# Optimization experiments

Hardware: AMD Instinct MI355X
Metric: run time of the kernel (lower is better)

## Reference

```python
import jax, jax.numpy as jnp
import numpy as np

D_MODEL = 1024
N_HEADS = 16
HEAD_DIM = D_MODEL // N_HEADS
FFN_DIM = 4096
N_EXPERTS = 8
CAP_FRAC = 0.25          # moe_eval_capacity_token_fraction (eval mode)
MOE_TOKEN_DROPOUT = 0.2  # eval: expert output scaled by (1 - p)
LN_EPS = 1e-5
B, S = 4, 512


def setup_inputs():
    key = jax.random.key(0)
    ks = jax.random.split(key, 20)
    def w(k, shape, scale=0.02):
        return jax.random.normal(k, shape, jnp.float32) * scale
    return {
        "x": jax.random.normal(ks[0], (B, S, D_MODEL), jnp.float32),
        "wq": w(ks[1], (D_MODEL, D_MODEL)), "bq": w(ks[2], (D_MODEL,)),
        "wk": w(ks[3], (D_MODEL, D_MODEL)), "bk": w(ks[4], (D_MODEL,)),
        "wv": w(ks[5], (D_MODEL, D_MODEL)), "bv": w(ks[6], (D_MODEL,)),
        "wo": w(ks[7], (D_MODEL, D_MODEL)), "bo": w(ks[8], (D_MODEL,)),
        "ln1_g": 1.0 + w(ks[9], (D_MODEL,)), "ln1_b": w(ks[10], (D_MODEL,)),
        "ln2_g": 1.0 + w(ks[11], (D_MODEL,)), "ln2_b": w(ks[12], (D_MODEL,)),
        "wr": w(ks[13], (D_MODEL, N_EXPERTS)),
        "w1": w(ks[14], (N_EXPERTS, D_MODEL, FFN_DIM)), "b1": w(ks[15], (N_EXPERTS, FFN_DIM)),
        "w2": w(ks[16], (N_EXPERTS, FFN_DIM, D_MODEL)), "b2": w(ks[17], (N_EXPERTS, D_MODEL)),
    }


def _layer_norm(x, g, b):
    mu = x.mean(-1, keepdims=True)
    var = ((x - mu) ** 2).mean(-1, keepdims=True)
    return (x - mu) * jax.lax.rsqrt(var + LN_EPS) * g + b


def _self_attention(x, wq, bq, wk, bk, wv, bv, wo, bo):
    b, s, d = x.shape
    q = ((x @ wq + bq) * (HEAD_DIM ** -0.5)).reshape(b, s, N_HEADS, HEAD_DIM)
    k = (x @ wk + bk).reshape(b, s, N_HEADS, HEAD_DIM)
    v = (x @ wv + bv).reshape(b, s, N_HEADS, HEAD_DIM)
    scores = jnp.einsum('bqhd,bkhd->bhqk', q, k)
    p = jax.nn.softmax(scores, axis=-1)
    o = jnp.einsum('bhqk,bkhd->bqhd', p, v).reshape(b, s, d)
    return o @ wo + bo


def _moe_ffn(x, wr, w1, b1, w2, b2):
    # x: [T, D]. NLLB-MoE top-2 router with capacity dropping (eval mode,
    # second_expert_policy='all', normalize_router_prob_before_dropping=False).
    T, D = x.shape
    C = int(np.ceil(CAP_FRAC * T))  # static expert capacity
    logits = x @ wr                                    # [T, E] router dtype fp32
    probs = jax.nn.softmax(logits, axis=-1)
    top1 = jnp.argmax(probs, axis=-1)                  # [T]
    m1 = jax.nn.one_hot(top1, N_EXPERTS, dtype=x.dtype)
    top2 = jnp.argmax(jnp.where(m1 > 0, -jnp.inf, logits), axis=-1)
    m2 = jax.nn.one_hot(top2, N_EXPERTS, dtype=x.dtype)
    loc1 = jnp.cumsum(m1, axis=0) - 1.0                # slot within expert
    loc2 = jnp.cumsum(m2, axis=0) - 1.0 + m1.sum(0, keepdims=True)
    m1 = m1 * (loc1 < C)                               # capacity dropping
    m2 = m2 * (loc2 < C)
    t1 = (probs * m1).sum(-1)
    t2 = (probs * m2).sum(-1)
    denom = jnp.maximum(t1 + t2, jnp.finfo(x.dtype).eps)
    t1, t2 = t1 / denom, t2 / denom
    tok = jnp.arange(T)
    s1 = loc1[tok, top1].astype(jnp.int32)
    s2 = loc2[tok, top2].astype(jnp.int32)
    v1 = m1[tok, top1] > 0
    v2 = m2[tok, top2] > 0
    s1 = jnp.where(v1, s1, C)  # out-of-range slot -> dropped by scatter
    s2 = jnp.where(v2, s2, C)
    # dispatch tokens to capacity buffers [E, C, D] (slots are unique)
    buf = jnp.zeros((N_EXPERTS, C, D), x.dtype)
    buf = buf.at[top1, s1].set(x, mode='drop')
    buf = buf.at[top2, s2].set(x, mode='drop')
    # grouped expert FFN (relu), eval-mode moe_token_dropout scaling
    h = jax.nn.relu(jnp.einsum('ecd,edf->ecf', buf, w1) + b1[:, None, :])
    y = (jnp.einsum('ecf,efd->ecd', h, w2) + b2[:, None, :]) * (1.0 - MOE_TOKEN_DROPOUT)
    # combine with normalized top-2 gates (dropped tokens get gate 0)
    y1 = y[top1, jnp.minimum(s1, C - 1)]
    y2 = y[top2, jnp.minimum(s2, C - 1)]
    g1 = t1 * v1
    g2 = t2 * v2
    return g1[:, None] * y1 + g2[:, None] * y2


def reference(x, wq, bq, wk, bk, wv, bv, wo, bo, ln1_g, ln1_b, ln2_g, ln2_b, wr, w1, b1, w2, b2):
    # Pre-LN self-attention block
    h = _layer_norm(x, ln1_g, ln1_b)
    h = _self_attention(h, wq, bq, wk, bk, wv, bv, wo, bo)
    x = x + h
    # Pre-LN sparse MoE FFN block
    h = _layer_norm(x, ln2_g, ln2_b)
    b, s, d = h.shape
    moe = _moe_ffn(h.reshape(b * s, d), wr, w1, b1, w2, b2).reshape(b, s, d)
    return x + moe
```

## Files before the change

kernel.cpp:

```cpp
#include <hip/hip_runtime.h>
#include <hip/hip_bf16.h>
#include <stdint.h>

#define T_TOK 2048
#define DM 1024
#define NHEAD 16
#define HDIM 64
#define SEQ 512
#define NEXP 8
#define FFN 4096
#define CAP 512
#define LN_EPSV 1e-5f
#define ROUTER_EPS 1.1920929e-07f

typedef __bf16 bf16x8 __attribute__((ext_vector_type(8)));
typedef float f32x4 __attribute__((ext_vector_type(4)));

__device__ __forceinline__ void gld_lds16(const __hip_bfloat16* g, __hip_bfloat16* l) {
  __builtin_amdgcn_global_load_lds(
      (const __attribute__((address_space(1))) void*)g,
      (__attribute__((address_space(3))) void*)l, 16, 0, 0);
}

__global__ void transpose_cvt(const float* __restrict__ W, __hip_bfloat16* __restrict__ WT,
                              int R, int Cc) {
  __shared__ float tile[32][33];
  int e = blockIdx.z;
  const float* src = W + (size_t)e * R * Cc;
  __hip_bfloat16* dst = WT + (size_t)e * R * Cc;
  int c0 = blockIdx.x * 32, r0 = blockIdx.y * 32;
  int tx = threadIdx.x, ty = threadIdx.y;
#pragma unroll
  for (int i = 0; i < 4; i++) {
    int r = r0 + ty + i * 8;
    tile[ty + i * 8][tx] = src[(size_t)r * Cc + c0 + tx];
  }
  __syncthreads();
#pragma unroll
  for (int i = 0; i < 4; i++) {
    int c = c0 + ty + i * 8;
    dst[(size_t)c * R + r0 + tx] = __float2bfloat16(tile[tx][ty + i * 8]);
  }
}

__global__ void transpose_cvt_hp(const float* __restrict__ W, __hip_bfloat16* __restrict__ WH,
                                 __hip_bfloat16* __restrict__ WL, int R, int Cc, float scale) {
  __shared__ float tile[32][33];
  int c0 = blockIdx.x * 32, r0 = blockIdx.y * 32;
  int tx = threadIdx.x, ty = threadIdx.y;
#pragma unroll
  for (int i = 0; i < 4; i++) {
    int r = r0 + ty + i * 8;
    tile[ty + i * 8][tx] = W[(size_t)r * Cc + c0 + tx];
  }
  __syncthreads();
#pragma unroll
  for (int i = 0; i < 4; i++) {
    int c = c0 + ty + i * 8;
    float v = tile[tx][ty + i * 8] * scale;
    __hip_bfloat16 h = __float2bfloat16(v);
    WH[(size_t)c * R + r0 + tx] = h;
    WL[(size_t)c * R + r0 + tx] = __float2bfloat16(v - __bfloat162float(h));
  }
}

__global__ __launch_bounds__(256) void pack_bias(const float* __restrict__ bq,
                                                 const float* __restrict__ bk,
                                                 const float* __restrict__ bv,
                                                 float* __restrict__ outp) {
  int t = blockIdx.x * 256 + threadIdx.x;
  if (t < DM) outp[t] = bq[t] * 0.125f;
  else if (t < 2 * DM) outp[t] = bk[t - DM];
  else if (t < 3 * DM) outp[t] = bv[t - 2 * DM];
}

__global__ __launch_bounds__(256) void ln1_hp(const float* __restrict__ x,
                                              const float* __restrict__ g,
                                              const float* __restrict__ bta,
                                              __hip_bfloat16* __restrict__ ohi,
                                              __hip_bfloat16* __restrict__ olo) {
  int row = blockIdx.x, t = threadIdx.x;
  const float4* xr = (const float4*)(x + (size_t)row * DM);
  float4 v = xr[t];
  float s = v.x + v.y + v.z + v.w;
  float ss = v.x * v.x + v.y * v.y + v.z * v.z + v.w * v.w;
  __shared__ float rs[4], rss[4];
  __shared__ float smu, sinv;
  int wid = t >> 6, lane = t & 63;
  for (int off = 32; off; off >>= 1) { s += __shfl_down(s, off); ss += __shfl_down(ss, off); }
  if (!lane) { rs[wid] = s; rss[wid] = ss; }
  __syncthreads();
  if (!t) {
    float S = rs[0] + rs[1] + rs[2] + rs[3], SS = rss[0] + rss[1] + rss[2] + rss[3];
    float mu = S / DM;
    float var = SS / DM - mu * mu;
    smu = mu; sinv = 1.0f / sqrtf(var + LN_EPSV);
  }
  __syncthreads();
  float mu = smu, inv = sinv;
  float4 gv = ((const float4*)g)[t], bv = ((const float4*)bta)[t];
  float n[4];
  n[0] = (v.x - mu) * inv * gv.x + bv.x;
  n[1] = (v.y - mu) * inv * gv.y + bv.y;
  n[2] = (v.z - mu) * inv * gv.z + bv.z;
  n[3] = (v.w - mu) * inv * gv.w + bv.w;
  __hip_bfloat16* hr = ohi + (size_t)row * DM + t * 4;
  __hip_bfloat16* lr = olo + (size_t)row * DM + t * 4;
#pragma unroll
  for (int k = 0; k < 4; k++) {
    __hip_bfloat16 h = __float2bfloat16(n[k]);
    hr[k] = h;
    lr[k] = __float2bfloat16(n[k] - __bfloat162float(h));
  }
}

__global__ __launch_bounds__(256) void cvt_hp(const float* __restrict__ in,
                                              __hip_bfloat16* __restrict__ hi,
                                              __hip_bfloat16* __restrict__ lo) {
  int i = (blockIdx.x * 256 + threadIdx.x) * 4;
  float4 v = *(const float4*)&in[i];
  float n[4] = {v.x, v.y, v.z, v.w};
#pragma unroll
  for (int k = 0; k < 4; k++) {
    __hip_bfloat16 h = __float2bfloat16(n[k]);
    hi[i + k] = h;
    lo[i + k] = __float2bfloat16(n[k] - __bfloat162float(h));
  }
}

template <int BM, int BN, int TM, int TN, bool BT>
__global__ __launch_bounds__(256) void gemm_f32(
    const float* __restrict__ A, const float* __restrict__ B, float* __restrict__ Cc,
    const float* __restrict__ bias, const float* __restrict__ resid,
    int M, int N, int K, int lda, int ldb, int ldc, float scale, int zdiv,
    long long sA1, long long sA2, long long sB1, long long sB2,
    long long sC1, long long sC2) {
  constexpr int BK = 16;
  __shared__ float As[BK][BM + 4];
  __shared__ float Bs[BK][BN + 4];
  int z = blockIdx.z;
  int zq = z / zdiv, zr = z % zdiv;
  A += zq * sA1 + zr * sA2;
  B += zq * sB1 + zr * sB2;
  Cc += zq * sC1 + zr * sC2;
  int tid = threadIdx.x;
  int m0 = blockIdx.y * BM, n0 = blockIdx.x * BN;
  constexpr int NTX = BN / TN;
  int tx = tid % NTX, ty = tid / NTX;
  float acc[TM][TN] = {};
  for (int k0 = 0; k0 < K; k0 += BK) {
    constexpr int ALOADS = BM * BK / (256 * 4);
#pragma unroll
    for (int i = 0; i < ALOADS; i++) {
      int idx = tid + i * 256;
      int m = idx / (BK / 4);
      int kk = (idx % (BK / 4)) * 4;
      float4 va = *(const float4*)&A[(size_t)(m0 + m) * lda + k0 + kk];
      As[kk + 0][m] = va.x; As[kk + 1][m] = va.y; As[kk + 2][m] = va.z; As[kk + 3][m] = va.w;
    }
    constexpr int BLOADS = BK * BN / (256 * 4);
    if (!BT) {
#pragma unroll
      for (int i = 0; i < BLOADS; i++) {
        int idx = tid + i * 256;
        int kk = idx / (BN / 4);
        int n = (idx % (BN / 4)) * 4;
        *(float4*)&Bs[kk][n] = *(const float4*)&B[(size_t)(k0 + kk) * ldb + n0 + n];
      }
    } else {
#pragma unroll
      for (int i = 0; i < BLOADS; i++) {
        int idx = tid + i * 256;
        int n = idx / (BK / 4);
        int kk = (idx % (BK / 4)) * 4;
        float4 vb = *(const float4*)&B[(size_t)(n0 + n) * ldb + k0 + kk];
        Bs[kk + 0][n] = vb.x; Bs[kk + 1][n] = vb.y; Bs[kk + 2][n] = vb.z; Bs[kk + 3][n] = vb.w;
      }
    }
    __syncthreads();
#pragma unroll
    for (int kk = 0; kk < BK; kk++) {
      float ar[TM], br[TN];
#pragma unroll
      for (int i = 0; i < TM; i += 4) *(float4*)&ar[i] = *(const float4*)&As[kk][ty * TM + i];
#pragma unroll
      for (int j = 0; j < TN; j += 4) *(float4*)&br[j] = *(const float4*)&Bs[kk][tx * TN + j];
#pragma unroll
      for (int i = 0; i < TM; i++)
#pragma unroll
        for (int j = 0; j < TN; j++) acc[i][j] += ar[i] * br[j];
    }
    __syncthreads();
  }
#pragma unroll
  for (int i = 0; i < TM; i++) {
    int m = m0 + ty * TM + i;
#pragma unroll
    for (int j = 0; j < TN; j++) {
      int n = n0 + tx * TN + j;
      float v = acc[i][j];
      if (bias) v += bias[n];
      v *= scale;
      if (resid) v += resid[(size_t)m * ldc + n];
      acc[i][j] = v;
    }
#pragma unroll
    for (int j = 0; j < TN; j += 4)
      *(float4*)&Cc[(size_t)m * ldc + n0 + tx * TN + j] = *(float4*)&acc[i][j];
  }
}

__global__ __launch_bounds__(256) void softmax_rows(float* __restrict__ sc) {
  int row = blockIdx.x, t = threadIdx.x;
  float* p = sc + (size_t)row * SEQ;
  float2 v = *(const float2*)&p[t * 2];
  float mx = fmaxf(v.x, v.y);
  __shared__ float r[4];
  __shared__ float bmax, bsum;
  int wid = t >> 6, lane = t & 63;
  for (int off = 32; off; off >>= 1) mx = fmaxf(mx, __shfl_down(mx, off));
  if (!lane) r[wid] = mx;
  __syncthreads();
  if (!t) bmax = fmaxf(fmaxf(r[0], r[1]), fmaxf(r[2], r[3]));
  __syncthreads();
  mx = bmax;
  float e0 = __expf(v.x - mx), e1v = __expf(v.y - mx);
  float s = e0 + e1v;
  for (int off = 32; off; off >>= 1) s += __shfl_down(s, off);
  if (!lane) r[wid] = s;
  __syncthreads();
  if (!t) bsum = r[0] + r[1] + r[2] + r[3];
  __syncthreads();
  float inv = 1.0f / bsum;
  float2 o; o.x = e0 * inv; o.y = e1v * inv;
  *(float2*)&p[t * 2] = o;
}

template <int MODE>
__global__ __launch_bounds__(256) void gemm_hp(
    const __hip_bfloat16* __restrict__ Ahi, const __hip_bfloat16* __restrict__ Alo,
    const __hip_bfloat16* __restrict__ Bhi, const __hip_bfloat16* __restrict__ Blo,
    float* __restrict__ Cc, const float* __restrict__ bias, const float* __restrict__ resid,
    int M, int N, int K, long long sB, long long sC, int biasStride) {
  constexpr int BM = 128, BN = 128, BK = 64;
  __shared__ __align__(16) __hip_bfloat16 AsH[BM * BK];
  __shared__ __align__(16) __hip_bfloat16 AsL[BM * BK];
  __shared__ __align__(16) __hip_bfloat16 BsH[BN * BK];
  __shared__ __align__(16) __hip_bfloat16 BsL[BN * BK];
  int e = blockIdx.z;
  Bhi += (size_t)e * sB; Blo += (size_t)e * sB;
  size_t czoff = (size_t)e * sC;
  const float* bvec = bias + (size_t)e * biasStride;
  int m0 = blockIdx.y * BM, n0 = blockIdx.x * BN;
  int tid = threadIdx.x;
  int lane = tid & 63, quad = lane >> 4, l16 = lane & 15, wv = tid >> 6;
  int wm = wv >> 1, wn = wv & 1;
  f32x4 acc[4][4] = {};
  for (int k0 = 0; k0 < K; k0 += BK) {
#pragma unroll
    for (int i = 0; i < 4; i++) {
      int flat = tid + i * 256;
      int r = flat >> 3, lc = flat & 7;
      int pc = lc ^ (r & 7);
      gld_lds16(Ahi + (size_t)(m0 + r) * K + k0 + pc * 8, AsH + flat * 8);
      gld_lds16(Alo + (size_t)(m0 + r) * K + k0 + pc * 8, AsL + flat * 8);
      gld_lds16(Bhi + (size_t)(n0 + r) * K + k0 + pc * 8, BsH + flat * 8);
      gld_lds16(Blo + (size_t)(n0 + r) * K + k0 + pc * 8, BsL + flat * 8);
    }
    __syncthreads();
#pragma unroll
    for (int ks = 0; ks < 2; ks++) {
      bf16x8 ah[4], al[4], bh[4], bl[4];
#pragma unroll
      for (int i = 0; i < 4; i++) {
        int r = wm * 64 + i * 16 + l16;
        int pc = (ks * 4 + quad) ^ (r & 7);
        ah[i] = *(const bf16x8*)(AsH + r * BK + pc * 8);
        al[i] = *(const bf16x8*)(AsL + r * BK + pc * 8);
      }
#pragma unroll
      for (int j = 0; j < 4; j++) {
        int r = wn * 64 + j * 16 + l16;
        int pc = (ks * 4 + quad) ^ (r & 7);
        bh[j] = *(const bf16x8*)(BsH + r * BK + pc * 8);
        bl[j] = *(const bf16x8*)(BsL + r * BK + pc * 8);
      }
#pragma unroll
      for (int i = 0; i < 4; i++)
#pragma unroll
        for (int j = 0; j < 4; j++) {
          acc[i][j] = __builtin_amdgcn_mfma_f32_16x16x32_bf16(ah[i], bh[j], acc[i][j], 0, 0, 0);
          acc[i][j] = __builtin_amdgcn_mfma_f32_16x16x32_bf16(ah[i], bl[j], acc[i][j], 0, 0, 0);
          acc[i][j] = __builtin_amdgcn_mfma_f32_16x16x32_bf16(al[i], bh[j], acc[i][j], 0, 0, 0);
        }
    }
    __syncthreads();
  }
#pragma unroll
  for (int j = 0; j < 4; j++) {
    int col = n0 + wn * 64 + j * 16 + l16;
    float bb = bvec[col];
#pragma unroll
    for (int i = 0; i < 4; i++) {
      int row0 = m0 + wm * 64 + i * 16 + quad * 4;
#pragma unroll
      for (int r = 0; r < 4; r++) {
        float v = acc[i][j][r] + bb;
        if (MODE == 3) v += resid[(size_t)(row0 + r) * N + col];
        Cc[czoff + (size_t)(row0 + r) * N + col] = v;
      }
    }
  }
}

__global__ __launch_bounds__(256) void ln2_router(const float* __restrict__ x2,
                                                  const float* __restrict__ g,
                                                  const float* __restrict__ bta,
                                                  const float* __restrict__ wr,
                                                  __hip_bfloat16* __restrict__ h2,
                                                  float* __restrict__ logits) {
  int row = blockIdx.x, t = threadIdx.x;
  const float4* xr = (const float4*)(x2 + (size_t)row * DM);
  float4 v = xr[t];
  float s = v.x + v.y + v.z + v.w;
  float ss = v.x * v.x + v.y * v.y + v.z * v.z + v.w * v.w;
  __shared__ float rs[4], rss[4];
  __shared__ float smu, sinv;
  int wid = t >> 6, lane = t & 63;
  for (int off = 32; off; off >>= 1) { s += __shfl_down(s, off); ss += __shfl_down(ss, off); }
  if (!lane) { rs[wid] = s; rss[wid] = ss; }
  __syncthreads();
  if (!t) {
    float S = rs[0] + rs[1] + rs[2] + rs[3], SS = rss[0] + rss[1] + rss[2] + rss[3];
    float mu = S / DM;
    float var = SS / DM - mu * mu;
    smu = mu; sinv = 1.0f / sqrtf(var + LN_EPSV);
  }
  __syncthreads();
  float mu = smu, inv = sinv;
  float4 gv = ((const float4*)g)[t], bv = ((const float4*)bta)[t];
  float n0 = (v.x - mu) * inv * gv.x + bv.x;
  float n1 = (v.y - mu) * inv * gv.y + bv.y;
  float n2 = (v.z - mu) * inv * gv.z + bv.z;
  float n3 = (v.w - mu) * inv * gv.w + bv.w;
  __hip_bfloat16* hr = h2 + (size_t)row * DM + t * 4;
  hr[0] = __float2bfloat16(n0); hr[1] = __float2bfloat16(n1);
  hr[2] = __float2bfloat16(n2); hr[3] = __float2bfloat16(n3);
  const float* w0 = wr + (size_t)(t * 4) * NEXP;
  __shared__ float red[256 * NEXP];
#pragma unroll
  for (int e = 0; e < NEXP; e++)
    red[t * NEXP + e] = n0 * w0[e] + n1 * w0[NEXP + e] + n2 * w0[2 * NEXP + e] + n3 * w0[3 * NEXP + e];
  __syncthreads();
  for (int sdt = 128; sdt > 0; sdt >>= 1) {
    if (t < sdt) {
#pragma unroll
      for (int e = 0; e < NEXP; e++) red[t * NEXP + e] += red[(t + sdt) * NEXP + e];
    }
    __syncthreads();
  }
  if (t < NEXP) logits[(size_t)row * NEXP + t] = red[t];
}

__global__ __launch_bounds__(256) void routing(const float* __restrict__ logits,
                                               int* __restrict__ e1o, int* __restrict__ s1o,
                                               float* __restrict__ g1o,
                                               int* __restrict__ e2o, int* __restrict__ s2o,
                                               float* __restrict__ g2o,
                                               int* __restrict__ src_tok) {
  __shared__ unsigned char t1s[T_TOK], t2s[T_TOK];
  __shared__ unsigned short r1s[T_TOK], r2s[T_TOK];
  __shared__ int cnt1s[NEXP];
  int t = threadIdx.x;
  for (int i = t; i < NEXP * CAP; i += 256) src_tok[i] = -1;
  for (int tok = t; tok < T_TOK; tok += 256) {
    float lg[NEXP];
#pragma unroll
    for (int e = 0; e < NEXP; e++) lg[e] = logits[(size_t)tok * NEXP + e];
    int b1 = 0; float m1v = lg[0];
#pragma unroll
    for (int e = 1; e < NEXP; e++) if (lg[e] > m1v) { m1v = lg[e]; b1 = e; }
    int b2 = -1; float m2v = -3.4e38f;
#pragma unroll
    for (int e = 0; e < NEXP; e++) if (e != b1 && lg[e] > m2v) { m2v = lg[e]; b2 = e; }
    t1s[tok] = (unsigned char)b1; t2s[tok] = (unsigned char)b2;
  }
  __syncthreads();
  if (t < 64) {
    int base[NEXP] = {0, 0, 0, 0, 0, 0, 0, 0};
    for (int c = 0; c < T_TOK / 64; c++) {
      int tok = c * 64 + t;
      int my = t1s[tok];
      unsigned long long below = (1ull << t) - 1ull;
#pragma unroll
      for (int e = 0; e < NEXP; e++) {
        unsigned long long msk = __ballot(my == e);
        if (my == e) r1s[tok] = (unsigned short)(base[e] + __popcll(msk & below));
        base[e] += (int)__popcll(msk);
      }
    }
    if (t == 0) {
#pragma unroll
      for (int e = 0; e < NEXP; e++) cnt1s[e] = base[e];
    }
#pragma unroll
    for (int e = 0; e < NEXP; e++) base[e] = 0;
    for (int c = 0; c < T_TOK / 64; c++) {
      int tok = c * 64 + t;
      int my = t2s[tok];
      unsigned long long below = (1ull << t) - 1ull;
#pragma unroll
      for (int e = 0; e < NEXP; e++) {
        unsigned long long msk = __ballot(my == e);
        if (my == e) r2s[tok] = (unsigned short)(base[e] + __popcll(msk & below));
        base[e] += (int)__popcll(msk);
      }
    }
  }
  __syncthreads();
  for (int tok = t; tok < T_TOK; tok += 256) {
    float lg[NEXP];
#pragma unroll
    for (int e = 0; e < NEXP; e++) lg[e] = logits[(size_t)tok * NEXP + e];
    int b1 = t1s[tok], b2 = t2s[tok];
    float lb1 = lg[0], lb2 = lg[0];
#pragma unroll
    for (int e = 0; e < NEXP; e++) { if (e == b1) lb1 = lg[e]; if (e == b2) lb2 = lg[e]; }
    float sum = 0.f;
#pragma unroll
    for (int e = 0; e < NEXP; e++) sum += __expf(lg[e] - lb1);
    float p1 = 1.0f / sum;
    float p2 = __expf(lb2 - lb1) / sum;
    int sl1 = r1s[tok];
    int sl2 = r2s[tok] + cnt1s[b2];
    bool v1 = sl1 < CAP, v2 = sl2 < CAP;
    float tt1 = v1 ? p1 : 0.f, tt2 = v2 ? p2 : 0.f;
    float den = fmaxf(tt1 + tt2, ROUTER_EPS);
    float gg1 = v1 ? tt1 / den : 0.f;
    float gg2 = v2 ? tt2 / den : 0.f;
    e1o[tok] = b1; s1o[tok] = v1 ? sl1 : 0; g1o[tok] = gg1;
    e2o[tok] = b2; s2o[tok] = v2 ? sl2 : 0; g2o[tok] = gg2;
    if (v1) src_tok[b1 * CAP + sl1] = tok;
    if (v2) src_tok[b2 * CAP + sl2] = tok;
  }
}

__global__ __launch_bounds__(64) void dispatch(const int* __restrict__ src_tok,
                                               const __hip_bfloat16* __restrict__ h2,
                                               __hip_bfloat16* __restrict__ Amoe) {
  int rowb = blockIdx.x, t = threadIdx.x;
  int tok = src_tok[rowb];
  uint4* dst = (uint4*)(Amoe + (size_t)rowb * DM);
  if (tok >= 0) {
    const uint4* src = (const uint4*)(h2 + (size_t)tok * DM);
    dst[t] = src[t]; dst[t + 64] = src[t + 64];
  } else {
    uint4 z = make_uint4(0, 0, 0, 0);
    dst[t] = z; dst[t + 64] = z;
  }
}

template <int MODE>
__global__ __launch_bounds__(256) void gemm_bf16(
    const __hip_bfloat16* __restrict__ A, const __hip_bfloat16* __restrict__ Bt,
    __hip_bfloat16* __restrict__ Cc, const float* __restrict__ bias,
    int M, int N, int K, long long sA, long long sB, long long sC, int biasStride) {
  constexpr int BM = 128, BN = 128, BK = 64;
  __shared__ __align__(16) __hip_bfloat16 Asm[BM * BK];
  __shared__ __align__(16) __hip_bfloat16 Bsm[BN * BK];
  int e = blockIdx.z;
  A += (size_t)e * sA; Bt += (size_t)e * sB; Cc += (size_t)e * sC;
  const float* bvec = bias + (size_t)e * biasStride;
  int m0 = blockIdx.y * BM, n0 = blockIdx.x * BN;
  int tid = threadIdx.x;
  int lane = tid & 63, quad = lane >> 4, l16 = lane & 15, wv = tid >> 6;
  int wm = wv >> 1, wn = wv & 1;
  f32x4 acc[4][4] = {};
  for (int k0 = 0; k0 < K; k0 += BK) {
#pragma unroll
    for (int i = 0; i < 4; i++) {
      int flat = tid + i * 256;
      int r = flat >> 3, lc = flat & 7;
      int pc = lc ^ (r & 7);
      gld_lds16(A + (size_t)(m0 + r) * K + k0 + pc * 8, Asm + flat * 8);
      gld_lds16(Bt + (size_t)(n0 + r) * K + k0 + pc * 8, Bsm + flat * 8);
    }
    __syncthreads();
#pragma unroll
    for (int ks = 0; ks < 2; ks++) {
      bf16x8 af[4], bfr[4];
#pragma unroll
      for (int i = 0; i < 4; i++) {
        int r = wm * 64 + i * 16 + l16;
        int pc = (ks * 4 + quad) ^ (r & 7);
        af[i] = *(const bf16x8*)(Asm + r * BK + pc * 8);
      }
#pragma unroll
      for (int j = 0; j < 4; j++) {
        int r = wn * 64 + j * 16 + l16;
        int pc = (ks * 4 + quad) ^ (r & 7);
        bfr[j] = *(const bf16x8*)(Bsm + r * BK + pc * 8);
      }
#pragma unroll
      for (int i = 0; i < 4; i++)
#pragma unroll
        for (int j = 0; j < 4; j++)
          acc[i][j] = __builtin_amdgcn_mfma_f32_16x16x32_bf16(af[i], bfr[j], acc[i][j], 0, 0, 0);
    }
    __syncthreads();
  }
#pragma unroll
  for (int j = 0; j < 4; j++) {
    int col = n0 + wn * 64 + j * 16 + l16;
    float bb = bvec[col];
#pragma unroll
    for (int i = 0; i < 4; i++) {
      int row0 = m0 + wm * 64 + i * 16 + quad * 4;
#pragma unroll
      for (int r = 0; r < 4; r++) {
        float v = acc[i][j][r] + bb;
        if (MODE == 0) v = fmaxf(v, 0.0f);
        else v *= 0.8f;
        Cc[(size_t)(row0 + r) * N + col] = __float2bfloat16(v);
      }
    }
  }
}

__global__ __launch_bounds__(64) void combine(const float* __restrict__ x2,
                                              const __hip_bfloat16* __restrict__ Y,
                                              const int* __restrict__ e1, const int* __restrict__ s1,
                                              const float* __restrict__ g1,
                                              const int* __restrict__ e2, const int* __restrict__ s2,
                                              const float* __restrict__ g2,
                                              float* __restrict__ out) {
  int tok = blockIdx.x, t = threadIdx.x;
  float gg1 = g1[tok], gg2 = g2[tok];
  const __hip_bfloat16* y1 = Y + ((size_t)e1[tok] * CAP + s1[tok]) * DM;
  const __hip_bfloat16* y2 = Y + ((size_t)e2[tok] * CAP + s2[tok]) * DM;
  const float* xr = x2 + (size_t)tok * DM;
  float* orow = out + (size_t)tok * DM;
#pragma unroll
  for (int j = 0; j < 4; j++) {
    int idx = t * 4 + j * 256;
    float4 vv = *(const float4*)&xr[idx];
    float4 r;
    r.x = vv.x + gg1 * __bfloat162float(y1[idx + 0]) + gg2 * __bfloat162float(y2[idx + 0]);
    r.y = vv.y + gg1 * __bfloat162float(y1[idx + 1]) + gg2 * __bfloat162float(y2[idx + 1]);
    r.z = vv.z + gg1 * __bfloat162float(y1[idx + 2]) + gg2 * __bfloat162float(y2[idx + 2]);
    r.w = vv.w + gg1 * __bfloat162float(y1[idx + 3]) + gg2 * __bfloat162float(y2[idx + 3]);
    *(float4*)&orow[idx] = r;
  }
}

extern "C" void kernel_launch(void* const* d_in, const int* in_sizes, int n_in,
                              void* d_out, int out_size, void* d_ws, size_t ws_size,
                              hipStream_t stream) {
  (void)in_sizes; (void)n_in; (void)out_size; (void)ws_size;
  const float* x    = (const float*)d_in[0];
  const float* wq   = (const float*)d_in[1];
  const float* bq   = (const float*)d_in[2];
  const float* wk   = (const float*)d_in[3];
  const float* bk   = (const float*)d_in[4];
  const float* wv   = (const float*)d_in[5];
  const float* bv   = (const float*)d_in[6];
  const float* wo   = (const float*)d_in[7];
  const float* bo   = (const float*)d_in[8];
  const float* ln1g = (const float*)d_in[9];
  const float* ln1b = (const float*)d_in[10];
  const float* ln2g = (const float*)d_in[11];
  const float* ln2b = (const float*)d_in[12];
  const float* wr   = (const float*)d_in[13];
  const float* w1   = (const float*)d_in[14];
  const float* b1   = (const float*)d_in[15];
  const float* w2   = (const float*)d_in[16];
  const float* b2   = (const float*)d_in[17];
  float* out = (float*)d_out;
  char* ws = (char*)d_ws;

  __hip_bfloat16* W1T  = (__hip_bfloat16*)(ws + 0);
  __hip_bfloat16* W2T  = (__hip_bfloat16*)(ws + 67108864);
  float* sc            = (float*)(ws + 134217728);
  __hip_bfloat16* h1hi = (__hip_bfloat16*)(ws + 134217728);
  __hip_bfloat16* h1lo = (__hip_bfloat16*)(ws + 138412032);
  float* bqkv          = (float*)(ws + 142606336);
  __hip_bfloat16* WQKVH= (__hip_bfloat16*)(ws + 143654912);
  __hip_bfloat16* WQKVL= (__hip_bfloat16*)(ws + 149946368);
  __hip_bfloat16* Hm   = (__hip_bfloat16*)(ws + 134217728);
  float* logits        = (float*)(ws + 167772160);
  int*   e1a           = (int*)(ws + 167837696);
  int*   s1a           = (int*)(ws + 167845888);
  int*   e2a           = (int*)(ws + 167854080);
  int*   s2a           = (int*)(ws + 167862272);
  float* g1a           = (float*)(ws + 167870464);
  float* g2a           = (float*)(ws + 167878656);
  int*   src_tok       = (int*)(ws + 167886848);
  float* qkv           = (float*)(ws + 201326592);
  float* q             = qkv;
  float* k_            = qkv + 2097152;
  float* v             = qkv + 4194304;
  float* o_f           = (float*)(ws + 201326592);
  float* x2            = (float*)(ws + 201326592);
  __hip_bfloat16* ohi  = (__hip_bfloat16*)(ws + 209715200);
  __hip_bfloat16* olo  = (__hip_bfloat16*)(ws + 213909504);
  __hip_bfloat16* Y    = (__hip_bfloat16*)(ws + 209715200);
  __hip_bfloat16* h2   = (__hip_bfloat16*)(ws + 218103808);
  __hip_bfloat16* Amoe = (__hip_bfloat16*)(ws + 222298112);
  __hip_bfloat16* WOH  = (__hip_bfloat16*)(ws + 226492416);
  __hip_bfloat16* WOL  = (__hip_bfloat16*)(ws + 228589568);

  transpose_cvt<<<dim3(FFN / 32, DM / 32, NEXP), dim3(32, 8), 0, stream>>>(w1, W1T, DM, FFN);
  transpose_cvt<<<dim3(DM / 32, FFN / 32, NEXP), dim3(32, 8), 0, stream>>>(w2, W2T, FFN, DM);
  transpose_cvt_hp<<<dim3(DM / 32, DM / 32, 1), dim3(32, 8), 0, stream>>>(
      wq, WQKVH, WQKVL, DM, DM, 0.125f);
  transpose_cvt_hp<<<dim3(DM / 32, DM / 32, 1), dim3(32, 8), 0, stream>>>(
      wk, WQKVH + (size_t)DM * DM, WQKVL + (size_t)DM * DM, DM, DM, 1.0f);
  transpose_cvt_hp<<<dim3(DM / 32, DM / 32, 1), dim3(32, 8), 0, stream>>>(
      wv, WQKVH + (size_t)2 * DM * DM, WQKVL + (size_t)2 * DM * DM, DM, DM, 1.0f);
  transpose_cvt_hp<<<dim3(DM / 32, DM / 32, 1), dim3(32, 8), 0, stream>>>(
      wo, WOH, WOL, DM, DM, 1.0f);
  pack_bias<<<3 * DM / 256, 256, 0, stream>>>(bq, bk, bv, bqkv);
  ln1_hp<<<T_TOK, 256, 0, stream>>>(x, ln1g, ln1b, h1hi, h1lo);
  gemm_hp<2><<<dim3(DM / 128, T_TOK / 128, 3), 256, 0, stream>>>(
      h1hi, h1lo, WQKVH, WQKVL, qkv, bqkv, nullptr, T_TOK, DM, DM,
      (long long)DM * DM, (long long)T_TOK * DM, DM);
  gemm_f32<128, 128, 8, 8, true><<<dim3(SEQ / 128, SEQ / 128, 64), 256, 0, stream>>>(
      q, k_, sc, nullptr, nullptr, SEQ, SEQ, HDIM, DM, DM, SEQ, 1.0f, NHEAD,
      (long long)SEQ * DM, HDIM, (long long)SEQ * DM, HDIM,
      (long long)NHEAD * SEQ * SEQ, (long long)SEQ * SEQ);
  softmax_rows<<<64 * SEQ, 256, 0, stream>>>(sc);
  gemm_f32<128, 64, 8, 4, false><<<dim3(1, SEQ / 128, 64), 256, 0, stream>>>(
      sc, v, o_f, nullptr, nullptr, SEQ, HDIM, SEQ, SEQ, DM, DM, 1.0f, NHEAD,
      (long long)NHEAD * SEQ * SEQ, (long long)SEQ * SEQ,
      (long long)SEQ * DM, HDIM, (long long)SEQ * DM, HDIM);
  cvt_hp<<<T_TOK * DM / 1024, 256, 0, stream>>>(o_f, ohi, olo);
  gemm_hp<3><<<dim3(DM / 128, T_TOK / 128, 1), 256, 0, stream>>>(
      ohi, olo, WOH, WOL, x2, bo, x, T_TOK, DM, DM, 0LL, 0LL, 0);
  ln2_router<<<T_TOK, 256, 0, stream>>>(x2, ln2g, ln2b, wr, h2, logits);
  routing<<<1, 256, 0, stream>>>(logits, e1a, s1a, g1a, e2a, s2a, g2a, src_tok);
  dispatch<<<NEXP * CAP, 64, 0, stream>>>(src_tok, h2, Amoe);
  gemm_bf16<0><<<dim3(FFN / 128, CAP / 128, NEXP), 256, 0, stream>>>(
      Amoe, W1T, Hm, b1, CAP, FFN, DM,
      (long long)CAP * DM, (long long)FFN * DM, (long long)CAP * FFN, FFN);
  gemm_bf16<1><<<dim3(DM / 128, CAP / 128, NEXP), 256, 0, stream>>>(
      Hm, W2T, Y, b2, CAP, DM, FFN,
      (long long)CAP * FFN, (long long)DM * FFN, (long long)CAP * DM, DM);
  combine<<<T_TOK, 64, 0, stream>>>(x2, Y, e1a, s1a, g1a, e2a, s2a, g2a, out);
}
```

Measured before the change: 757.4 us.

## Double-buffer LDS tiles in GEMM kernels and remap workgroups across XCDs

Both GEMM kernels now stage tiles into two LDS buffers, issuing the next K-tile's global-to-LDS loads before the MFMAs on the current tile, with one barrier per iteration. The split-bf16 kernel halves BK to 32 so the doubled buffers keep the same LDS footprint, and gets a new swizzle for the narrower rows. A workgroup-index remap spreads consecutive tiles by XCD so neighbouring tiles share L2. The aim is to hide global-load latency and improve cache locality, at the cost of more barriers per K in the hp kernel and a remap that assumes the workgroup count is divisible by 8.

```diff
diff --git a/kernel.cpp b/kernel.cpp
--- a/kernel.cpp
+++ b/kernel.cpp
@@ -20,6 +20,19 @@
   __builtin_amdgcn_global_load_lds(
       (const __attribute__((address_space(1))) void*)g,
       (__attribute__((address_space(3))) void*)l, 16, 0, 0);
+}
+
+__device__ __forceinline__ void xcd_remap(int& bx, int& by, int& bz) {
+  int gx = gridDim.x, gy = gridDim.y, gz = gridDim.z;
+  int nwg = gx * gy * gz;
+  int lin = (blockIdx.z * gy + blockIdx.y) * gx + blockIdx.x;
+  int q = nwg >> 3;
+  int lin2 = (lin & 7) * q + (lin >> 3);
+  int gxy = gx * gy;
+  bz = lin2 / gxy;
+  int rem = lin2 - bz * gxy;
+  by = rem / gx;
+  bx = rem - by * gx;
 }
 
 __global__ void transpose_cvt(const float* __restrict__ W, __hip_bfloat16* __restrict__ WT,
@@ -242,58 +255,63 @@
     const __hip_bfloat16* __restrict__ Bhi, const __hip_bfloat16* __restrict__ Blo,
     float* __restrict__ Cc, const float* __restrict__ bias, const float* __restrict__ resid,
     int M, int N, int K, long long sB, long long sC, int biasStride) {
-  constexpr int BM = 128, BN = 128, BK = 64;
-  __shared__ __align__(16) __hip_bfloat16 AsH[BM * BK];
-  __shared__ __align__(16) __hip_bfloat16 AsL[BM * BK];
-  __shared__ __align__(16) __hip_bfloat16 BsH[BN * BK];
-  __shared__ __align__(16) __hip_bfloat16 BsL[BN * BK];
-  int e = blockIdx.z;
+  constexpr int BM = 128, BN = 128, BK = 32;
+  __shared__ __align__(16) __hip_bfloat16 AsH[2][BM * BK];
+  __shared__ __align__(16) __hip_bfloat16 AsL[2][BM * BK];
+  __shared__ __align__(16) __hip_bfloat16 BsH[2][BN * BK];
+  __shared__ __align__(16) __hip_bfloat16 BsL[2][BN * BK];
+  int bx, by, bz;
+  xcd_remap(bx, by, bz);
+  int e = bz;
   Bhi += (size_t)e * sB; Blo += (size_t)e * sB;
   size_t czoff = (size_t)e * sC;
   const float* bvec = bias + (size_t)e * biasStride;
-  int m0 = blockIdx.y * BM, n0 = blockIdx.x * BN;
+  int m0 = by * BM, n0 = bx * BN;
   int tid = threadIdx.x;
   int lane = tid & 63, quad = lane >> 4, l16 = lane & 15, wv = tid >> 6;
   int wm = wv >> 1, wn = wv & 1;
   f32x4 acc[4][4] = {};
-  for (int k0 = 0; k0 < K; k0 += BK) {
+  auto STAGE = [&](int buf, int k0) {
+#pragma unroll
+    for (int i = 0; i < 2; i++) {
+      int flat = tid + i * 256;
+      int r = flat >> 2, lc = flat & 3;
+      int pc = lc ^ ((r >> 1) & 3);
+      gld_lds16(Ahi + (size_t)(m0 + r) * K + k0 + pc * 8, &AsH[buf][flat * 8]);
+      gld_lds16(Alo + (size_t)(m0 + r) * K + k0 + pc * 8, &AsL[buf][flat * 8]);
+      gld_lds16(Bhi + (size_t)(n0 + r) * K + k0 + pc * 8, &BsH[buf][flat * 8]);
+      gld_lds16(Blo + (size_t)(n0 + r) * K + k0 + pc * 8, &BsL[buf][flat * 8]);
+    }
+  };
+  STAGE(0, 0);
+  __syncthreads();
+  int KT = K / BK;
+  for (int kt = 0; kt < KT; kt++) {
+    int cur = kt & 1;
+    if (kt + 1 < KT) STAGE(cur ^ 1, (kt + 1) * BK);
+    bf16x8 ah[4], al[4], bh[4], bl[4];
 #pragma unroll
     for (int i = 0; i < 4; i++) {
-      int flat = tid + i * 256;
-      int r = flat >> 3, lc = flat & 7;
-      int pc = lc ^ (r & 7);
-      gld_lds16(Ahi + (size_t)(m0 + r) * K + k0 + pc * 8, AsH + flat * 8);
-      gld_lds16(Alo + (size_t)(m0 + r) * K + k0 + pc * 8, AsL + flat * 8);
-      gld_lds16(Bhi + (size_t)(n0 + r) * K + k0 + pc * 8, BsH + flat * 8);
-      gld_lds16(Blo + (size_t)(n0 + r) * K + k0 + pc * 8, BsL + flat * 8);
-    }
-    __syncthreads();
-#pragma unroll
-    for (int ks = 0; ks < 2; ks++) {
-      bf16x8 ah[4], al[4], bh[4], bl[4];
-#pragma unroll
-      for (int i = 0; i < 4; i++) {
-        int r = wm * 64 + i * 16 + l16;
-        int pc = (ks * 4 + quad) ^ (r & 7);
-        ah[i] = *(const bf16x8*)(AsH + r * BK + pc * 8);
-        al[i] = *(const bf16x8*)(AsL + r * BK + pc * 8);
-      }
+      int r = wm * 64 + i * 16 + l16;
+      int pc = quad ^ ((r >> 1) & 3);
+      ah[i] = *(const bf16x8*)(&AsH[cur][r * BK + pc * 8]);
+      al[i] = *(const bf16x8*)(&AsL[cur][r * BK + pc * 8]);
+    }
+#pragma unroll
+    for (int j = 0; j < 4; j++) {
+      int r = wn * 64 + j * 16 + l16;
+      int pc = quad ^ ((r >> 1) & 3);
+      bh[j] = *(const bf16x8*)(&BsH[cur][r * BK + pc * 8]);
+      bl[j] = *(const bf16x8*)(&BsL[cur][r * BK + pc * 8]);
+    }
+#pragma unroll
+    for (int i = 0; i < 4; i++)
 #pragma unroll
       for (int j = 0; j < 4; j++) {
-        int r = wn * 64 + j * 16 + l16;
-        int pc = (ks * 4 + quad) ^ (r & 7);
-        bh[j] = *(const bf16x8*)(BsH + r * BK + pc * 8);
-        bl[j] = *(const bf16x8*)(BsL + r * BK + pc * 8);
-      }
-#pragma unroll
-      for (int i = 0; i < 4; i++)
-#pragma unroll
-        for (int j = 0; j < 4; j++) {
-          acc[i][j] = __builtin_amdgcn_mfma_f32_16x16x32_bf16(ah[i], bh[j], acc[i][j], 0, 0, 0);
-          acc[i][j] = __builtin_amdgcn_mfma_f32_16x16x32_bf16(ah[i], bl[j], acc[i][j], 0, 0, 0);
-          acc[i][j] = __builtin_amdgcn_mfma_f32_16x16x32_bf16(al[i], bh[j], acc[i][j], 0, 0, 0);
-        }
-    }
+        acc[i][j] = __builtin_amdgcn_mfma_f32_16x16x32_bf16(ah[i], bh[j], acc[i][j], 0, 0, 0);
+        acc[i][j] = __builtin_amdgcn_mfma_f32_16x16x32_bf16(ah[i], bl[j], acc[i][j], 0, 0, 0);
+        acc[i][j] = __builtin_amdgcn_mfma_f32_16x16x32_bf16(al[i], bh[j], acc[i][j], 0, 0, 0);
+      }
     __syncthreads();
   }
 #pragma unroll
@@ -466,26 +484,34 @@
     __hip_bfloat16* __restrict__ Cc, const float* __restrict__ bias,
     int M, int N, int K, long long sA, long long sB, long long sC, int biasStride) {
   constexpr int BM = 128, BN = 128, BK = 64;
-  __shared__ __align__(16) __hip_bfloat16 Asm[BM * BK];
-  __shared__ __align__(16) __hip_bfloat16 Bsm[BN * BK];
-  int e = blockIdx.z;
+  __shared__ __align__(16) __hip_bfloat16 Asm[2][BM * BK];
+  __shared__ __align__(16) __hip_bfloat16 Bsm[2][BN * BK];
+  int bx, by, bz;
+  xcd_remap(bx, by, bz);
+  int e = bz;
   A += (size_t)e * sA; Bt += (size_t)e * sB; Cc += (size_t)e * sC;
   const float* bvec = bias + (size_t)e * biasStride;
-  int m0 = blockIdx.y * BM, n0 = blockIdx.x * BN;
+  int m0 = by * BM, n0 = bx * BN;
   int tid = threadIdx.x;
   int lane = tid & 63, quad = lane >> 4, l16 = lane & 15, wv = tid >> 6;
   int wm = wv >> 1, wn = wv & 1;
   f32x4 acc[4][4] = {};
-  for (int k0 = 0; k0 < K; k0 += BK) {
+  auto STAGE = [&](int buf, int k0) {
 #pragma unroll
     for (int i = 0; i < 4; i++) {
       int flat = tid + i * 256;
       int r = flat >> 3, lc = flat & 7;
       int pc = lc ^ (r & 7);
-      gld_lds16(A + (size_t)(m0 + r) * K + k0 + pc * 8, Asm + flat * 8);
-      gld_lds16(Bt + (size_t)(n0 + r) * K + k0 + pc * 8, Bsm + flat * 8);
-    }
-    __syncthreads();
+      gld_lds16(A + (size_t)(m0 + r) * K + k0 + pc * 8, &Asm[buf][flat * 8]);
+      gld_lds16(Bt + (size_t)(n0 + r) * K + k0 + pc * 8, &Bsm[buf][flat * 8]);
+    }
+  };
+  STAGE(0, 0);
+  __syncthreads();
+  int KT = K / BK;
+  for (int kt = 0; kt < KT; kt++) {
+    int cur = kt & 1;
+    if (kt + 1 < KT) STAGE(cur ^ 1, (kt + 1) * BK);
 #pragma unroll
     for (int ks = 0; ks < 2; ks++) {
       bf16x8 af[4], bfr[4];
@@ -493,13 +519,13 @@
       for (int i = 0; i < 4; i++) {
         int r = wm * 64 + i * 16 + l16;
         int pc = (ks * 4 + quad) ^ (r & 7);
-        af[i] = *(const bf16x8*)(Asm + r * BK + pc * 8);
+        af[i] = *(const bf16x8*)(&Asm[cur][r * BK + pc * 8]);
       }
 #pragma unroll
       for (int j = 0; j < 4; j++) {
         int r = wn * 64 + j * 16 + l16;
         int pc = (ks * 4 + quad) ^ (r & 7);
-        bfr[j] = *(const bf16x8*)(Bsm + r * BK + pc * 8);
+        bfr[j] = *(const bf16x8*)(&Bsm[cur][r * BK + pc * 8]);
       }
 #pragma unroll
       for (int i = 0; i < 4; i++)
```

Result: no change. 760.9 us (+0.5%).
